# Kernel optimization log

Measured on AMD Instinct MI355X. Metric: run time of the kernel, lower is better.

## Reference

```python
import jax, jax.numpy as jnp
import numpy as np

H = 0.1  # spatial delta h from init kwargs


def _stencils():
    k_avg = jnp.array([[0., 0., 0.], [0., 1., 0.], [0., 0., 0.]], jnp.float32)
    k_x = (0.5 / H) * jnp.array([[0., -1., 0.], [0., 0., 0.], [0., 1., 0.]], jnp.float32)
    k_y = (0.5 / H) * jnp.array([[0., 0., 0.], [-1., 0., 1.], [0., 0., 0.]], jnp.float32)
    k_xx = (1.0 / H ** 2) * jnp.array([[0., 1., 0.], [0., -2., 0.], [0., 1., 0.]], jnp.float32)
    k_yy = (1.0 / H ** 2) * jnp.array([[0., 0., 0.], [1., -2., 1.], [0., 0., 0.]], jnp.float32)
    return k_avg, k_x, k_y, k_xx, k_yy


def setup_inputs() -> dict:
    key = jax.random.key(0)
    ks = jax.random.split(key, 11)
    B = 65536
    inp = {
        'data': jax.random.normal(ks[0], (B, 3, 11, 11), jnp.float32),
        'mix_a': jax.random.normal(ks[1], (128, 5 * 3 * 81), jnp.float32),
        'mix_b': jax.random.normal(ks[2], (128,), jnp.float32),
        'w1': jax.random.normal(ks[3], (128, 128), jnp.float32) * 0.08,
        'b1': jax.random.normal(ks[4], (128,), jnp.float32) * 0.05,
        'w2': jax.random.normal(ks[5], (128, 128), jnp.float32) * 0.08,
        'b2': jax.random.normal(ks[6], (128,), jnp.float32) * 0.05,
        'w3': jax.random.normal(ks[7], (128, 128), jnp.float32) * 0.08,
        'b3': jax.random.normal(ks[8], (128,), jnp.float32) * 0.05,
        'wf': jax.random.normal(ks[9], (5, 128), jnp.float32) * 0.08,
        'bf': jax.random.normal(ks[10], (5,), jnp.float32) * 0.05,
    }
    return inp


def reference(data, mix_a, mix_b, w1, b1, w2, b2, w3, b3, wf, bf):
    b = data.shape[0]
    # 3x3 patches over the 11x11 grid -> (b, c, 3, 3, 9, 9); last two dims are the
    # 9x9 valid output positions (l = n*9+m, matching torch unfold's reshape order).
    patches = jnp.stack(
        [jnp.stack([data[:, :, i:i + 9, j:j + 9] for j in range(3)], axis=2)
         for i in range(3)], axis=2)
    feats = [jnp.einsum('bcijnm,ij->bcnm', patches, k).reshape(b, -1)
             for k in _stencils()]  # each (b, 3*81)
    mixed = jnp.concatenate(feats, axis=1) @ mix_a.T + mix_b  # (b, 128)
    x = jnp.tanh(mixed)
    x = jnp.tanh(x @ w1.T + b1)
    x = jnp.tanh(x @ w2.T + b2)
    x = jnp.tanh(x @ w3.T + b3)
    return x @ wf.T + bf  # (b, 5)
```

## Files before the change

### kernel.cpp

```cpp
#include <hip/hip_runtime.h>
#include <hip/hip_bf16.h>

typedef __attribute__((ext_vector_type(4))) float f32x4;
typedef __attribute__((ext_vector_type(8))) short bf16x8;

#define MFMA(a,b,c) __builtin_amdgcn_mfma_f32_16x16x32_bf16((a),(b),(c),0,0,0)

__device__ inline void split_bf16(float a, unsigned short &h, unsigned short &l) {
    unsigned u = __float_as_uint(a);
    unsigned rh = (u + 0x7FFFu + ((u >> 16) & 1u)) & 0xFFFF0000u;
    float hf = __uint_as_float(rh);
    h = (unsigned short)(rh >> 16);
    float lf = a - hf;
    unsigned u2 = __float_as_uint(lf);
    l = (unsigned short)((u2 + 0x7FFFu + ((u2 >> 16) & 1u)) >> 16);
}

__device__ inline unsigned short bf16_rn(float a) {
    unsigned u = __float_as_uint(a);
    return (unsigned short)((u + 0x7FFFu + ((u >> 16) & 1u)) >> 16);
}

__device__ inline float tanh_fast(float x) {
    float e = __expf(2.f * x);
    return 1.f - 2.f * __builtin_amdgcn_rcpf(e + 1.f);
}

__device__ inline bf16x8 ldb(const unsigned short* p) { return *(const bf16x8*)p; }
__device__ inline f32x4 ld4u(const float* p) { f32x4 v; __builtin_memcpy(&v, p, 16); return v; }

__global__ void prep_all(const float* __restrict__ mix_a,
                         const float* __restrict__ w1, const float* __restrict__ w2,
                         const float* __restrict__ w3, const float* __restrict__ wf,
                         unsigned short* __restrict__ wph, unsigned short* __restrict__ wpl,
                         unsigned short* __restrict__ wlh, unsigned short* __restrict__ wfh) {
    int idx = blockIdx.x * 256 + threadIdx.x;
    if (idx < 128 * 384) {
        int o = idx / 384;
        int k = idx - o * 384;
        float acc = 0.f;
        if (k < 363) {
            int c = k / 121, rem = k - c * 121;
            int y = rem / 11, x = rem - y * 11;
            const float* ma = mix_a + (size_t)o * 1215 + c * 81;
            auto add = [&](int f, int i, int j, float coef) {
                int n = y - i, m = x - j;
                if (n >= 0 && n < 9 && m >= 0 && m < 9)
                    acc += ma[f * 243 + n * 9 + m] * coef;
            };
            add(0, 1, 1, 1.f);
            add(1, 0, 1, -5.f);  add(1, 2, 1, 5.f);
            add(2, 1, 0, -5.f);  add(2, 1, 2, 5.f);
            add(3, 0, 1, 100.f); add(3, 1, 1, -200.f); add(3, 2, 1, 100.f);
            add(4, 1, 0, 100.f); add(4, 1, 1, -200.f); add(4, 1, 2, 100.f);
        }
        unsigned short h, l; split_bf16(acc, h, l);
        int kt = k >> 5, ot = o >> 4;
        int lane = (o & 15) + 16 * ((k >> 3) & 3);
        int pidx = ((kt * 8 + ot) * 64 + lane) * 8 + (k & 7);
        wph[pidx] = h; wpl[pidx] = l;
        return;
    }
    idx -= 128 * 384;
    if (idx < 3 * 16384) {
        int layer = idx >> 14; int rem = idx & 16383;
        int o = rem >> 7, k = rem & 127;
        const float* w = (layer == 0) ? w1 : ((layer == 1) ? w2 : w3);
        float v = w[o * 128 + k];
        int kt = k >> 5, ot = o >> 4;
        int lane = (o & 15) + 16 * ((k >> 3) & 3);
        int pidx = layer * 16384 + ((kt * 8 + ot) * 64 + lane) * 8 + (k & 7);
        wlh[pidx] = bf16_rn(v);
    } else if (idx < 3 * 16384 + 2048) {
        int rem = idx - 3 * 16384;
        int o = rem >> 7, k = rem & 127;
        float v = (o < 5) ? wf[o * 128 + k] : 0.f;
        int kt = k >> 5;
        int lane = (o & 15) + 16 * ((k >> 3) & 3);
        int pidx = (kt * 64 + lane) * 8 + (k & 7);
        wfh[pidx] = bf16_rn(v);
    }
}

__global__ __launch_bounds__(256, 4)
void fused_main(const float* __restrict__ data,
                const float* __restrict__ mix_b,
                const float* __restrict__ b1v,
                const float* __restrict__ b2v,
                const float* __restrict__ b3v,
                const float* __restrict__ bfv,
                const unsigned short* __restrict__ wp1h,
                const unsigned short* __restrict__ wp1l,
                const unsigned short* __restrict__ wlh,
                const unsigned short* __restrict__ wfh,
                float* __restrict__ out, int Btot) {
    __shared__ __align__(16) unsigned short XsH[4][16][136];

    const int wave = threadIdx.x >> 6;
    const int lane = threadIdx.x & 63;
    const int s0 = (blockIdx.x * 4 + wave) * 16;
    if (s0 >= Btot) return;
    const int col = lane & 15;
    const int kg  = lane >> 4;

    const float* arow = data + (size_t)(s0 + col) * 363;

    f32x4 acc[8];
    #pragma unroll
    for (int ot = 0; ot < 8; ++ot) {
        float b = mix_b[col + 16 * ot];
        acc[ot] = (f32x4){b, b, b, b};
    }

    bf16x8 bh[8];
    f32x4 a4[2][2];
    a4[0][0] = ld4u(arow + kg * 8);
    a4[0][1] = ld4u(arow + kg * 8 + 4);

    #pragma unroll
    for (int ktg = 0; ktg < 12; ++ktg) {
        const int p = ktg & 1;
        #pragma unroll
        for (int ot = 0; ot < 8; ++ot)
            bh[ot] = ldb(wp1h + (((size_t)(ktg * 8 + ot)) * 64 + lane) * 8);
        if (ktg < 10) {
            const int kb = (ktg + 1) * 32 + kg * 8;
            a4[p ^ 1][0] = ld4u(arow + kb);
            a4[p ^ 1][1] = ld4u(arow + kb + 4);
        } else if (ktg == 10) {
            #pragma unroll
            for (int i = 0; i < 2; ++i)
                #pragma unroll
                for (int j = 0; j < 4; ++j) {
                    int k = 352 + kg * 8 + i * 4 + j;
                    bool ok = (k < 363);
                    a4[p ^ 1][i][j] = ok ? arow[k] : 0.f;
                }
        }
        bf16x8 ah, al;
        #pragma unroll
        for (int i = 0; i < 2; ++i)
            #pragma unroll
            for (int j = 0; j < 4; ++j) {
                unsigned short hh, ll;
                split_bf16(a4[p][i][j], hh, ll);
                ah[i * 4 + j] = (short)hh;
                al[i * 4 + j] = (short)ll;
            }
        #pragma unroll
        for (int ot = 0; ot < 8; ++ot)
            acc[ot] = MFMA(ah, bh[ot], acc[ot]);
        #pragma unroll
        for (int ot = 0; ot < 8; ++ot)
            acc[ot] = MFMA(al, bh[ot], acc[ot]);
        #pragma unroll
        for (int ot = 0; ot < 8; ++ot) {
            bf16x8 bl = ldb(wp1l + (((size_t)(ktg * 8 + ot)) * 64 + lane) * 8);
            acc[ot] = MFMA(ah, bl, acc[ot]);
        }
    }

    bf16x8 lbh[2][8];
    #pragma unroll
    for (int ot = 0; ot < 8; ++ot)
        lbh[0][ot] = ldb(wlh + ((size_t)ot * 64 + lane) * 8);

    #pragma unroll
    for (int ot = 0; ot < 8; ++ot)
        #pragma unroll
        for (int j = 0; j < 4; ++j)
            XsH[wave][kg * 4 + j][col + 16 * ot] = bf16_rn(tanh_fast(acc[ot][j]));

    const float* biases[3] = {b1v, b2v, b3v};
    asm volatile("s_waitcnt lgkmcnt(0)" ::: "memory");

    #pragma unroll
    for (int layer = 0; layer < 3; ++layer) {
        const float* bb = biases[layer];
        f32x4 nacc[8];
        #pragma unroll
        for (int ot = 0; ot < 8; ++ot) {
            float b = bb[col + 16 * ot];
            nacc[ot] = (f32x4){b, b, b, b};
        }
        #pragma unroll
        for (int kt = 0; kt < 4; ++kt) {
            const int s = layer * 4 + kt;
            const int p = s & 1;
            if (s < 11) {
                const int nl = (s + 1) >> 2, nk = (s + 1) & 3;
                const unsigned short* ph = wlh + (size_t)nl * 16384;
                #pragma unroll
                for (int ot = 0; ot < 8; ++ot)
                    lbh[p ^ 1][ot] = ldb(ph + (((size_t)(nk * 8 + ot)) * 64 + lane) * 8);
            }
            bf16x8 xh = *(const bf16x8*)&XsH[wave][col][kt * 32 + kg * 8];
            #pragma unroll
            for (int ot = 0; ot < 8; ++ot)
                nacc[ot] = MFMA(xh, lbh[p][ot], nacc[ot]);
        }
        asm volatile("s_waitcnt lgkmcnt(0)" ::: "memory");
        #pragma unroll
        for (int ot = 0; ot < 8; ++ot)
            #pragma unroll
            for (int j = 0; j < 4; ++j)
                XsH[wave][kg * 4 + j][col + 16 * ot] = bf16_rn(tanh_fast(nacc[ot][j]));
        asm volatile("s_waitcnt lgkmcnt(0)" ::: "memory");
    }

    float fb = (col < 5) ? bfv[col] : 0.f;
    f32x4 facc = (f32x4){fb, fb, fb, fb};
    #pragma unroll
    for (int kt = 0; kt < 4; ++kt) {
        bf16x8 fh = ldb(wfh + ((size_t)kt * 64 + lane) * 8);
        bf16x8 xh = *(const bf16x8*)&XsH[wave][col][kt * 32 + kg * 8];
        facc = MFMA(xh, fh, facc);
    }
    if (col < 5) {
        #pragma unroll
        for (int j = 0; j < 4; ++j) {
            int s = s0 + kg * 4 + j;
            if (s < Btot) out[(size_t)s * 5 + col] = facc[j];
        }
    }
}

extern "C" void kernel_launch(void* const* d_in, const int* in_sizes, int n_in,
                              void* d_out, int out_size, void* d_ws, size_t ws_size,
                              hipStream_t stream) {
    const float* data  = (const float*)d_in[0];
    const float* mix_a = (const float*)d_in[1];
    const float* mix_b = (const float*)d_in[2];
    const float* w1    = (const float*)d_in[3];
    const float* b1    = (const float*)d_in[4];
    const float* w2    = (const float*)d_in[5];
    const float* b2    = (const float*)d_in[6];
    const float* w3    = (const float*)d_in[7];
    const float* b3    = (const float*)d_in[8];
    const float* wf    = (const float*)d_in[9];
    const float* bf    = (const float*)d_in[10];
    float* out = (float*)d_out;
    int Btot = in_sizes[0] / 363;

    if (ws_size < 299008) return;
    unsigned short* wp1h = (unsigned short*)d_ws;
    unsigned short* wp1l = wp1h + 49152;
    unsigned short* wlh  = wp1l + 49152;
    unsigned short* wfh  = wlh + 49152;

    prep_all<<<392, 256, 0, stream>>>(mix_a, w1, w2, w3, wf,
                                      wp1h, wp1l, wlh, wfh);
    int blocks = (Btot + 63) / 64;
    fused_main<<<blocks, 256, 0, stream>>>(data, mix_b, b1, b2, b3, bf,
                                           wp1h, wp1l, wlh, wfh, out, Btot);
}
```

Before: 204.9 us.

## Stage packed weight tiles in shared memory cooperatively across the block's waves

Rather than having each of the four waves load every packed weight fragment from global memory on its own, the block now loads each 32-wide K slice of the mixing and hidden-layer weights once into LDS and double-buffers the next slice through registers. This removes the fourfold redundant global and L2 weight traffic. The cost is two block-wide barriers per K step, which also couple the waves. The early return for out-of-range tiles is replaced by clamping the data row so that every wave still reaches the barriers.

```diff
diff --git a/kernel.cpp b/kernel.cpp
--- a/kernel.cpp
+++ b/kernel.cpp
@@ -94,35 +94,52 @@
                 const unsigned short* __restrict__ wlh,
                 const unsigned short* __restrict__ wfh,
                 float* __restrict__ out, int Btot) {
+    __shared__ __align__(16) unsigned short BstH[4096];
+    __shared__ __align__(16) unsigned short BstL[4096];
     __shared__ __align__(16) unsigned short XsH[4][16][136];
 
-    const int wave = threadIdx.x >> 6;
-    const int lane = threadIdx.x & 63;
-    const int s0 = (blockIdx.x * 4 + wave) * 16;
-    if (s0 >= Btot) return;
-    const int col = lane & 15;
-    const int kg  = lane >> 4;
-
-    const float* arow = data + (size_t)(s0 + col) * 363;
-
+    const int t    = threadIdx.x;
+    const int wave = t >> 6;
+    const int lane = t & 63;
+    const int col  = lane & 15;
+    const int kg   = lane >> 4;
+    const int s0   = blockIdx.x * 64 + wave * 16;
+
+    int arowi = s0 + col;
+    if (arowi >= Btot) arowi = (Btot > 0) ? (Btot - 1) : 0;
+    const float* arow = data + (size_t)arowi * 363;
+
+    {
+        bf16x8 h0 = ldb(wp1h + t * 8);
+        bf16x8 h1 = ldb(wp1h + 2048 + t * 8);
+        bf16x8 l0 = ldb(wp1l + t * 8);
+        bf16x8 l1 = ldb(wp1l + 2048 + t * 8);
+        *(bf16x8*)&BstH[t * 8] = h0;  *(bf16x8*)&BstH[2048 + t * 8] = h1;
+        *(bf16x8*)&BstL[t * 8] = l0;  *(bf16x8*)&BstL[2048 + t * 8] = l1;
+    }
     f32x4 acc[8];
     #pragma unroll
     for (int ot = 0; ot < 8; ++ot) {
         float b = mix_b[col + 16 * ot];
         acc[ot] = (f32x4){b, b, b, b};
     }
-
-    bf16x8 bh[8];
     f32x4 a4[2][2];
     a4[0][0] = ld4u(arow + kg * 8);
     a4[0][1] = ld4u(arow + kg * 8 + 4);
-
+    __syncthreads();
+
+    bf16x8 pre0, pre1, pre2, pre3;
     #pragma unroll
     for (int ktg = 0; ktg < 12; ++ktg) {
         const int p = ktg & 1;
-        #pragma unroll
-        for (int ot = 0; ot < 8; ++ot)
-            bh[ot] = ldb(wp1h + (((size_t)(ktg * 8 + ot)) * 64 + lane) * 8);
+        if (ktg < 11) {
+            const unsigned short* nh = wp1h + (size_t)(ktg + 1) * 4096;
+            const unsigned short* nl = wp1l + (size_t)(ktg + 1) * 4096;
+            pre0 = ldb(nh + t * 8); pre1 = ldb(nh + 2048 + t * 8);
+            pre2 = ldb(nl + t * 8); pre3 = ldb(nl + 2048 + t * 8);
+        } else {
+            pre0 = ldb(wlh + t * 8); pre1 = ldb(wlh + 2048 + t * 8);
+        }
         if (ktg < 10) {
             const int kb = (ktg + 1) * 32 + kg * 8;
             a4[p ^ 1][0] = ld4u(arow + kb);
@@ -148,32 +165,34 @@
                 al[i * 4 + j] = (short)ll;
             }
         #pragma unroll
-        for (int ot = 0; ot < 8; ++ot)
-            acc[ot] = MFMA(ah, bh[ot], acc[ot]);
-        #pragma unroll
-        for (int ot = 0; ot < 8; ++ot)
-            acc[ot] = MFMA(al, bh[ot], acc[ot]);
-        #pragma unroll
         for (int ot = 0; ot < 8; ++ot) {
-            bf16x8 bl = ldb(wp1l + (((size_t)(ktg * 8 + ot)) * 64 + lane) * 8);
+            bf16x8 bh = *(const bf16x8*)&BstH[(ot * 64 + lane) * 8];
+            acc[ot] = MFMA(ah, bh, acc[ot]);
+            acc[ot] = MFMA(al, bh, acc[ot]);
+        }
+        #pragma unroll
+        for (int ot = 0; ot < 8; ++ot) {
+            bf16x8 bl = *(const bf16x8*)&BstL[(ot * 64 + lane) * 8];
             acc[ot] = MFMA(ah, bl, acc[ot]);
         }
-    }
-
-    bf16x8 lbh[2][8];
-    #pragma unroll
-    for (int ot = 0; ot < 8; ++ot)
-        lbh[0][ot] = ldb(wlh + ((size_t)ot * 64 + lane) * 8);
-
-    #pragma unroll
-    for (int ot = 0; ot < 8; ++ot)
-        #pragma unroll
-        for (int j = 0; j < 4; ++j)
-            XsH[wave][kg * 4 + j][col + 16 * ot] = bf16_rn(tanh_fast(acc[ot][j]));
+        if (ktg == 11) {
+            #pragma unroll
+            for (int ot = 0; ot < 8; ++ot)
+                #pragma unroll
+                for (int j = 0; j < 4; ++j)
+                    XsH[wave][kg * 4 + j][col + 16 * ot] = bf16_rn(tanh_fast(acc[ot][j]));
+        }
+        __syncthreads();
+        *(bf16x8*)&BstH[t * 8] = pre0;
+        *(bf16x8*)&BstH[2048 + t * 8] = pre1;
+        if (ktg < 11) {
+            *(bf16x8*)&BstL[t * 8] = pre2;
+            *(bf16x8*)&BstL[2048 + t * 8] = pre3;
+        }
+        __syncthreads();
+    }
 
     const float* biases[3] = {b1v, b2v, b3v};
-    asm volatile("s_waitcnt lgkmcnt(0)" ::: "memory");
-
     #pragma unroll
     for (int layer = 0; layer < 3; ++layer) {
         const float* bb = biases[layer];
@@ -186,20 +205,23 @@
         #pragma unroll
         for (int kt = 0; kt < 4; ++kt) {
             const int s = layer * 4 + kt;
-            const int p = s & 1;
             if (s < 11) {
-                const int nl = (s + 1) >> 2, nk = (s + 1) & 3;
-                const unsigned short* ph = wlh + (size_t)nl * 16384;
-                #pragma unroll
-                for (int ot = 0; ot < 8; ++ot)
-                    lbh[p ^ 1][ot] = ldb(ph + (((size_t)(nk * 8 + ot)) * 64 + lane) * 8);
+                const unsigned short* nsl = wlh + (size_t)(s + 1) * 4096;
+                pre0 = ldb(nsl + t * 8); pre1 = ldb(nsl + 2048 + t * 8);
+            } else {
+                pre0 = ldb(wfh + t * 8);
             }
             bf16x8 xh = *(const bf16x8*)&XsH[wave][col][kt * 32 + kg * 8];
             #pragma unroll
-            for (int ot = 0; ot < 8; ++ot)
-                nacc[ot] = MFMA(xh, lbh[p][ot], nacc[ot]);
-        }
-        asm volatile("s_waitcnt lgkmcnt(0)" ::: "memory");
+            for (int ot = 0; ot < 8; ++ot) {
+                bf16x8 bh = *(const bf16x8*)&BstH[(ot * 64 + lane) * 8];
+                nacc[ot] = MFMA(xh, bh, nacc[ot]);
+            }
+            __syncthreads();
+            *(bf16x8*)&BstH[t * 8] = pre0;
+            if (s < 11) *(bf16x8*)&BstH[2048 + t * 8] = pre1;
+            __syncthreads();
+        }
         #pragma unroll
         for (int ot = 0; ot < 8; ++ot)
             #pragma unroll
@@ -212,7 +234,7 @@
     f32x4 facc = (f32x4){fb, fb, fb, fb};
     #pragma unroll
     for (int kt = 0; kt < 4; ++kt) {
-        bf16x8 fh = ldb(wfh + ((size_t)kt * 64 + lane) * 8);
+        bf16x8 fh = *(const bf16x8*)&BstH[(kt * 64 + lane) * 8];
         bf16x8 xh = *(const bf16x8*)&XsH[wave][col][kt * 32 + kg * 8];
         facc = MFMA(xh, fh, facc);
     }
```

After: 186.0 us. -9.2%, faster.

## Stage weights in shared memory and process two row tiles per wave

Applied to the files above, without the earlier changes.

Weight tiles for the first mixing layer and the MLP layers are now loaded cooperatively by the block into double-buffered LDS, with register prefetch of the next tile and block-level barriers between steps. Previously each wave read all weights straight from global memory. Each wave also handles 32 samples instead of 16, so every B fragment read from LDS feeds two MFMAs, which halves weight traffic per sample. The cost is more registers (launch bounds lowered to 2 blocks per SM), a __syncthreads per k-step, and more LDS use, all of which lower occupancy.

```diff
diff --git a/kernel.cpp b/kernel.cpp
--- a/kernel.cpp
+++ b/kernel.cpp
@@ -82,7 +82,7 @@
     }
 }
 
-__global__ __launch_bounds__(256, 4)
+__global__ __launch_bounds__(256, 2)
 void fused_main(const float* __restrict__ data,
                 const float* __restrict__ mix_b,
                 const float* __restrict__ b1v,
@@ -94,134 +94,177 @@
                 const unsigned short* __restrict__ wlh,
                 const unsigned short* __restrict__ wfh,
                 float* __restrict__ out, int Btot) {
-    __shared__ __align__(16) unsigned short XsH[4][16][136];
-
-    const int wave = threadIdx.x >> 6;
-    const int lane = threadIdx.x & 63;
-    const int s0 = (blockIdx.x * 4 + wave) * 16;
-    if (s0 >= Btot) return;
-    const int col = lane & 15;
-    const int kg  = lane >> 4;
-
-    const float* arow = data + (size_t)(s0 + col) * 363;
-
-    f32x4 acc[8];
+    __shared__ __align__(16) unsigned short BstH[2][4096];
+    __shared__ __align__(16) unsigned short BstL[2][4096];
+    __shared__ __align__(16) unsigned short XsH[4][2][16][136];
+
+    const int t    = threadIdx.x;
+    const int wave = t >> 6;
+    const int lane = t & 63;
+    const int col  = lane & 15;
+    const int kg   = lane >> 4;
+    const int s0   = blockIdx.x * 128 + wave * 32;
+
+    int r0 = s0 + col, r1 = s0 + 16 + col;
+    if (r0 >= Btot) r0 = Btot - 1;
+    if (r1 >= Btot) r1 = Btot - 1;
+    const float* arow0 = data + (size_t)r0 * 363;
+    const float* arow1 = data + (size_t)r1 * 363;
+
+    bf16x8 pH0 = ldb(wp1h + t * 8), pH1 = ldb(wp1h + 2048 + t * 8);
+    bf16x8 pL0 = ldb(wp1l + t * 8), pL1 = ldb(wp1l + 2048 + t * 8);
+
+    f32x4 acc[2][8];
     #pragma unroll
     for (int ot = 0; ot < 8; ++ot) {
         float b = mix_b[col + 16 * ot];
-        acc[ot] = (f32x4){b, b, b, b};
-    }
-
-    bf16x8 bh[8];
-    f32x4 a4[2][2];
-    a4[0][0] = ld4u(arow + kg * 8);
-    a4[0][1] = ld4u(arow + kg * 8 + 4);
-
-    #pragma unroll
-    for (int ktg = 0; ktg < 12; ++ktg) {
-        const int p = ktg & 1;
-        #pragma unroll
-        for (int ot = 0; ot < 8; ++ot)
-            bh[ot] = ldb(wp1h + (((size_t)(ktg * 8 + ot)) * 64 + lane) * 8);
-        if (ktg < 10) {
-            const int kb = (ktg + 1) * 32 + kg * 8;
-            a4[p ^ 1][0] = ld4u(arow + kb);
-            a4[p ^ 1][1] = ld4u(arow + kb + 4);
-        } else if (ktg == 10) {
+        acc[0][ot] = (f32x4){b, b, b, b};
+        acc[1][ot] = (f32x4){b, b, b, b};
+    }
+    f32x4 a4[2][2][2];
+    a4[0][0][0] = ld4u(arow0 + kg * 8);  a4[0][0][1] = ld4u(arow0 + kg * 8 + 4);
+    a4[0][1][0] = ld4u(arow1 + kg * 8);  a4[0][1][1] = ld4u(arow1 + kg * 8 + 4);
+
+    *(bf16x8*)&BstH[0][t * 8] = pH0;  *(bf16x8*)&BstH[0][2048 + t * 8] = pH1;
+    *(bf16x8*)&BstL[0][t * 8] = pL0;  *(bf16x8*)&BstL[0][2048 + t * 8] = pL1;
+    pH0 = ldb(wp1h + 4096 + t * 8); pH1 = ldb(wp1h + 4096 + 2048 + t * 8);
+    pL0 = ldb(wp1l + 4096 + t * 8); pL1 = ldb(wp1l + 4096 + 2048 + t * 8);
+    __syncthreads();
+
+    #pragma unroll
+    for (int u = 0; u < 12; ++u) {
+        const int cur = u & 1;
+        *(bf16x8*)&BstH[cur ^ 1][t * 8] = pH0;
+        *(bf16x8*)&BstH[cur ^ 1][2048 + t * 8] = pH1;
+        if (u < 11) {
+            *(bf16x8*)&BstL[cur ^ 1][t * 8] = pL0;
+            *(bf16x8*)&BstL[cur ^ 1][2048 + t * 8] = pL1;
+        }
+        if (u < 10) {
+            const unsigned short* nh = wp1h + (size_t)(u + 2) * 4096;
+            const unsigned short* nl = wp1l + (size_t)(u + 2) * 4096;
+            pH0 = ldb(nh + t * 8); pH1 = ldb(nh + 2048 + t * 8);
+            pL0 = ldb(nl + t * 8); pL1 = ldb(nl + 2048 + t * 8);
+        } else {
+            const unsigned short* nh = wlh + (size_t)(u - 10) * 4096;
+            pH0 = ldb(nh + t * 8); pH1 = ldb(nh + 2048 + t * 8);
+        }
+        if (u < 10) {
+            const int kb = (u + 1) * 32 + kg * 8;
+            a4[cur ^ 1][0][0] = ld4u(arow0 + kb); a4[cur ^ 1][0][1] = ld4u(arow0 + kb + 4);
+            a4[cur ^ 1][1][0] = ld4u(arow1 + kb); a4[cur ^ 1][1][1] = ld4u(arow1 + kb + 4);
+        } else if (u == 10) {
             #pragma unroll
             for (int i = 0; i < 2; ++i)
                 #pragma unroll
                 for (int j = 0; j < 4; ++j) {
                     int k = 352 + kg * 8 + i * 4 + j;
                     bool ok = (k < 363);
-                    a4[p ^ 1][i][j] = ok ? arow[k] : 0.f;
+                    a4[cur ^ 1][0][i][j] = ok ? arow0[k] : 0.f;
+                    a4[cur ^ 1][1][i][j] = ok ? arow1[k] : 0.f;
                 }
         }
-        bf16x8 ah, al;
+        bf16x8 ah0, al0, ah1, al1;
         #pragma unroll
         for (int i = 0; i < 2; ++i)
             #pragma unroll
             for (int j = 0; j < 4; ++j) {
                 unsigned short hh, ll;
-                split_bf16(a4[p][i][j], hh, ll);
-                ah[i * 4 + j] = (short)hh;
-                al[i * 4 + j] = (short)ll;
-            }
+                split_bf16(a4[cur][0][i][j], hh, ll);
+                ah0[i * 4 + j] = (short)hh; al0[i * 4 + j] = (short)ll;
+                split_bf16(a4[cur][1][i][j], hh, ll);
+                ah1[i * 4 + j] = (short)hh; al1[i * 4 + j] = (short)ll;
+            }
+        #pragma unroll
+        for (int ot = 0; ot < 8; ++ot) {
+            bf16x8 bh = *(const bf16x8*)&BstH[cur][(ot * 64 + lane) * 8];
+            acc[0][ot] = MFMA(ah0, bh, acc[0][ot]);
+            acc[1][ot] = MFMA(ah1, bh, acc[1][ot]);
+            acc[0][ot] = MFMA(al0, bh, acc[0][ot]);
+            acc[1][ot] = MFMA(al1, bh, acc[1][ot]);
+        }
+        #pragma unroll
+        for (int ot = 0; ot < 8; ++ot) {
+            bf16x8 bl = *(const bf16x8*)&BstL[cur][(ot * 64 + lane) * 8];
+            acc[0][ot] = MFMA(ah0, bl, acc[0][ot]);
+            acc[1][ot] = MFMA(ah1, bl, acc[1][ot]);
+        }
+        __syncthreads();
+    }
+
+    #pragma unroll
+    for (int tt = 0; tt < 2; ++tt)
         #pragma unroll
         for (int ot = 0; ot < 8; ++ot)
-            acc[ot] = MFMA(ah, bh[ot], acc[ot]);
-        #pragma unroll
-        for (int ot = 0; ot < 8; ++ot)
-            acc[ot] = MFMA(al, bh[ot], acc[ot]);
-        #pragma unroll
-        for (int ot = 0; ot < 8; ++ot) {
-            bf16x8 bl = ldb(wp1l + (((size_t)(ktg * 8 + ot)) * 64 + lane) * 8);
-            acc[ot] = MFMA(ah, bl, acc[ot]);
-        }
-    }
-
-    bf16x8 lbh[2][8];
-    #pragma unroll
-    for (int ot = 0; ot < 8; ++ot)
-        lbh[0][ot] = ldb(wlh + ((size_t)ot * 64 + lane) * 8);
-
-    #pragma unroll
-    for (int ot = 0; ot < 8; ++ot)
-        #pragma unroll
-        for (int j = 0; j < 4; ++j)
-            XsH[wave][kg * 4 + j][col + 16 * ot] = bf16_rn(tanh_fast(acc[ot][j]));
+            #pragma unroll
+            for (int j = 0; j < 4; ++j)
+                XsH[wave][tt][kg * 4 + j][col + 16 * ot] = bf16_rn(tanh_fast(acc[tt][ot][j]));
+    asm volatile("s_waitcnt lgkmcnt(0)" ::: "memory");
 
     const float* biases[3] = {b1v, b2v, b3v};
-    asm volatile("s_waitcnt lgkmcnt(0)" ::: "memory");
-
     #pragma unroll
     for (int layer = 0; layer < 3; ++layer) {
         const float* bb = biases[layer];
-        f32x4 nacc[8];
+        f32x4 nacc[2][8];
         #pragma unroll
         for (int ot = 0; ot < 8; ++ot) {
             float b = bb[col + 16 * ot];
-            nacc[ot] = (f32x4){b, b, b, b};
+            nacc[0][ot] = (f32x4){b, b, b, b};
+            nacc[1][ot] = (f32x4){b, b, b, b};
         }
         #pragma unroll
         for (int kt = 0; kt < 4; ++kt) {
-            const int s = layer * 4 + kt;
-            const int p = s & 1;
-            if (s < 11) {
-                const int nl = (s + 1) >> 2, nk = (s + 1) & 3;
-                const unsigned short* ph = wlh + (size_t)nl * 16384;
+            const int u = 12 + layer * 4 + kt;
+            const int cur = u & 1;
+            *(bf16x8*)&BstH[cur ^ 1][t * 8] = pH0;
+            if (u < 23) *(bf16x8*)&BstH[cur ^ 1][2048 + t * 8] = pH1;
+            if (u < 22) {
+                const unsigned short* nh = wlh + (size_t)(u - 10) * 4096;
+                pH0 = ldb(nh + t * 8); pH1 = ldb(nh + 2048 + t * 8);
+            } else if (u == 22) {
+                pH0 = ldb(wfh + t * 8);
+            }
+            bf16x8 xh0 = *(const bf16x8*)&XsH[wave][0][col][kt * 32 + kg * 8];
+            bf16x8 xh1 = *(const bf16x8*)&XsH[wave][1][col][kt * 32 + kg * 8];
+            #pragma unroll
+            for (int ot = 0; ot < 8; ++ot) {
+                bf16x8 bh = *(const bf16x8*)&BstH[cur][(ot * 64 + lane) * 8];
+                nacc[0][ot] = MFMA(xh0, bh, nacc[0][ot]);
+                nacc[1][ot] = MFMA(xh1, bh, nacc[1][ot]);
+            }
+            __syncthreads();
+        }
+        asm volatile("s_waitcnt lgkmcnt(0)" ::: "memory");
+        #pragma unroll
+        for (int tt = 0; tt < 2; ++tt)
+            #pragma unroll
+            for (int ot = 0; ot < 8; ++ot)
                 #pragma unroll
-                for (int ot = 0; ot < 8; ++ot)
-                    lbh[p ^ 1][ot] = ldb(ph + (((size_t)(nk * 8 + ot)) * 64 + lane) * 8);
-            }
-            bf16x8 xh = *(const bf16x8*)&XsH[wave][col][kt * 32 + kg * 8];
-            #pragma unroll
-            for (int ot = 0; ot < 8; ++ot)
-                nacc[ot] = MFMA(xh, lbh[p][ot], nacc[ot]);
-        }
+                for (int j = 0; j < 4; ++j)
+                    XsH[wave][tt][kg * 4 + j][col + 16 * ot] = bf16_rn(tanh_fast(nacc[tt][ot][j]));
         asm volatile("s_waitcnt lgkmcnt(0)" ::: "memory");
-        #pragma unroll
-        for (int ot = 0; ot < 8; ++ot)
-            #pragma unroll
-            for (int j = 0; j < 4; ++j)
-                XsH[wave][kg * 4 + j][col + 16 * ot] = bf16_rn(tanh_fast(nacc[ot][j]));
-        asm volatile("s_waitcnt lgkmcnt(0)" ::: "memory");
     }
 
     float fb = (col < 5) ? bfv[col] : 0.f;
-    f32x4 facc = (f32x4){fb, fb, fb, fb};
+    f32x4 facc[2];
+    facc[0] = (f32x4){fb, fb, fb, fb};
+    facc[1] = (f32x4){fb, fb, fb, fb};
     #pragma unroll
     for (int kt = 0; kt < 4; ++kt) {
-        bf16x8 fh = ldb(wfh + ((size_t)kt * 64 + lane) * 8);
-        bf16x8 xh = *(const bf16x8*)&XsH[wave][col][kt * 32 + kg * 8];
-        facc = MFMA(xh, fh, facc);
+        bf16x8 fh = *(const bf16x8*)&BstH[0][(kt * 64 + lane) * 8];
+        bf16x8 xh0 = *(const bf16x8*)&XsH[wave][0][col][kt * 32 + kg * 8];
+        bf16x8 xh1 = *(const bf16x8*)&XsH[wave][1][col][kt * 32 + kg * 8];
+        facc[0] = MFMA(xh0, fh, facc[0]);
+        facc[1] = MFMA(xh1, fh, facc[1]);
     }
     if (col < 5) {
         #pragma unroll
-        for (int j = 0; j < 4; ++j) {
-            int s = s0 + kg * 4 + j;
-            if (s < Btot) out[(size_t)s * 5 + col] = facc[j];
-        }
+        for (int tt = 0; tt < 2; ++tt)
+            #pragma unroll
+            for (int j = 0; j < 4; ++j) {
+                int s = s0 + 16 * tt + kg * 4 + j;
+                if (s < Btot) out[(size_t)s * 5 + col] = facc[tt][j];
+            }
     }
 }
 
@@ -250,7 +293,7 @@
 
     prep_all<<<392, 256, 0, stream>>>(mix_a, w1, w2, w3, wf,
                                       wp1h, wp1l, wlh, wfh);
-    int blocks = (Btot + 63) / 64;
+    int blocks = (Btot + 127) / 128;
     fused_main<<<blocks, 256, 0, stream>>>(data, mix_b, b1, b2, b3, bf,
                                            wp1h, wp1l, wlh, wfh, out, Btot);
 }
```

After: 188.1 us. -8.2%, faster.
